# Optimization experiments

Measured on AMD Instinct MI355X. Metric: run time of the kernel, lower is better.

Reference implementation:

```python
import jax, jax.numpy as jnp
import numpy as np

T, B, E, H, HID, SIG = 1024, 4, 1024, 16, 1024, 64


def setup_inputs() -> dict:
    key = jax.random.key(0)
    ks = jax.random.split(key, 16)
    sc = 0.02
    return {
        "x": jax.random.normal(ks[0], (T, B, E), jnp.float32),
        "Wq": jax.random.normal(ks[1], (E, E), jnp.float32) * sc,
        "bq": jnp.zeros((E,), jnp.float32),
        "Wk": jax.random.normal(ks[2], (E, E), jnp.float32) * sc,
        "bk": jnp.zeros((E,), jnp.float32),
        "Wv": jax.random.normal(ks[3], (E, E), jnp.float32) * sc,
        "bv": jnp.zeros((E,), jnp.float32),
        "Wo": jax.random.normal(ks[4], (E, E), jnp.float32) * sc,
        "bo": jnp.zeros((E,), jnp.float32),
        "W1": jax.random.normal(ks[5], (HID, E), jnp.float32) * sc,
        "b1": jnp.zeros((HID,), jnp.float32),
        "W2": jax.random.normal(ks[6], (SIG, HID), jnp.float32) * sc,
        "b2": jnp.zeros((SIG,), jnp.float32),
        "head_signatures": jax.random.normal(ks[7], (H, SIG), jnp.float32),
    }


def reference(x, Wq, bq, Wk, bk, Wv, bv, Wo, bo, W1, b1, W2, b2, head_signatures):
    # x: (T, B, E) fairseq layout; self-attention, no mask, eval mode (no dropout)
    T_, B_, E_ = x.shape
    H_ = head_signatures.shape[0]
    d = E_ // H_
    scaling = d ** -0.5

    q = (x @ Wq.T + bq) * scaling            # (T,B,E)
    k = x @ Wk.T + bk
    v = x @ Wv.T + bv

    def split_heads(z):                        # (T,B,E) -> (B,H,T,d)
        return z.reshape(T_, B_, H_, d).transpose(1, 2, 0, 3)

    qh, kh, vh = split_heads(q), split_heads(k), split_heads(v)

    scores = jnp.einsum("bhtd,bhsd->bhts", qh, kh)   # (B,H,T,T)
    attn = jax.nn.softmax(scores, axis=-1)
    o = jnp.einsum("bhts,bhsd->bhtd", attn, vh)      # (B,H,T,d)

    # head-competition gate: signature MLP on x, match against head signatures,
    # softmax over heads ('softmax' competition type)
    t = jax.nn.relu(x @ W1.T + b1) @ W2.T + b2       # (T,B,SIG)
    logits = t @ head_signatures.T                   # (T,B,H)
    gate = jax.nn.softmax(logits, axis=-1)
    gate = gate.transpose(1, 2, 0)                   # (B,H,T)

    o = o * gate[..., None]                          # gate per-head outputs
    out = o.transpose(2, 0, 1, 3).reshape(T_, B_, E_)  # (T,B,E)
    return out @ Wo.T + bo
```

## Files before the change

### kernel.cpp

```cpp
#include <hip/hip_runtime.h>

#define Tn   1024
#define Bn   4
#define En   1024
#define Hn   16
#define HIDn 1024
#define SIGn 64
#define Mn   (Tn * Bn)

typedef short  s8x8  __attribute__((ext_vector_type(8)));
typedef float  f32x4 __attribute__((ext_vector_type(4)));

__device__ __forceinline__ unsigned short f2bf(float f) {
    unsigned int x = __float_as_uint(f);
    unsigned int r = (x + 0x7fffu + ((x >> 16) & 1u)) >> 16;
    return (unsigned short)r;
}
__device__ __forceinline__ float exp2asm(float x) {
    float r;
    asm("v_exp_f32 %0, %1" : "=v"(r) : "v"(x));
    return r;
}
__device__ __forceinline__ unsigned int cvtpk(float a, float b) {
    unsigned int r;
    asm("v_cvt_pk_bf16_f32 %0, %1, %2" : "=v"(r) : "v"(a), "v"(b));
    return r;
}

__device__ __forceinline__ void gload_lds16(const void* g, void* l) {
    __builtin_amdgcn_global_load_lds(
        (const __attribute__((address_space(1))) unsigned int*)g,
        (__attribute__((address_space(3))) unsigned int*)l, 16, 0, 0);
}

__device__ __forceinline__ void cast8(const float* s, unsigned short* d) {
    const float4* p = (const float4*)s;
    float4 a = p[0], b = p[1];
    s8x8 o;
    o[0] = (short)f2bf(a.x); o[1] = (short)f2bf(a.y);
    o[2] = (short)f2bf(a.z); o[3] = (short)f2bf(a.w);
    o[4] = (short)f2bf(b.x); o[5] = (short)f2bf(b.y);
    o[6] = (short)f2bf(b.z); o[7] = (short)f2bf(b.w);
    *(s8x8*)d = o;
}

__global__ __launch_bounds__(256) void prep_all(
    const float* __restrict__ x,  const float* __restrict__ W1,
    const float* __restrict__ Wq, const float* __restrict__ Wk,
    const float* __restrict__ Wv, const float* __restrict__ W2,
    const float* __restrict__ b1, const float* __restrict__ bq,
    const float* __restrict__ bk, const float* __restrict__ bv,
    unsigned short* __restrict__ Wcat, unsigned short* __restrict__ W2b,
    float* __restrict__ bcat, unsigned short* __restrict__ xb, int pre)
{
    const size_t WELEM = (size_t)En * En;
    const int y = blockIdx.y, bx = blockIdx.x, tid = threadIdx.x;
    if (y < 4) {
        const float* src = (y == 0) ? W1 : (y == 1) ? Wq : (y == 2) ? Wk : Wv;
        size_t i = (size_t)bx * 256 + tid;
        cast8(src + i * 8, Wcat + y * WELEM + i * 8);
    } else if (y == 4) {
        if (bx < 32) {
            size_t i = (size_t)bx * 256 + tid;
            cast8(W2 + i * 8, W2b + i * 8);
        } else if (bx < 48) {
            int idx = (bx - 32) * 256 + tid;
            int w = idx >> 10;
            const float* s = (w == 0) ? b1 : (w == 1) ? bq : (w == 2) ? bk : bv;
            bcat[idx] = s[idx & 1023];
        }
    } else {
        if (!pre) return;
        int q = y - 5;
        size_t i = (size_t)bx * 256 + tid;
        cast8(x + q * WELEM + i * 8, xb + q * WELEM + i * 8);
    }
}

template <int PRE>
__global__ __launch_bounds__(256) void fused_proj(
    const float* __restrict__ X, const unsigned short* __restrict__ Xb,
    const unsigned short* __restrict__ Wcat, const float* __restrict__ bcat,
    unsigned short* __restrict__ t1b, unsigned short* __restrict__ qb,
    unsigned short* __restrict__ kb, unsigned short* __restrict__ vb)
{
    __shared__ __align__(16) short As[128 * 32];
    __shared__ __align__(16) short Bs[128 * 32];
    const int tid  = threadIdx.x;
    const int wave = tid >> 6;
    const int lane = tid & 63;
    const int ln15 = lane & 15;
    const int kq   = lane >> 4;
    const int wr   = wave >> 1;
    const int wc   = wave & 1;
    const int bn   = blockIdx.x;
    const int bm   = blockIdx.y;
    const size_t rowA0 = (size_t)bm * 128;
    const size_t rowB0 = (size_t)bn * 128;

    const int lrow   = lane >> 2;
    const int lchunk = lane & 3;

    f32x4 acc[4][4];
#pragma unroll
    for (int m = 0; m < 4; m++)
#pragma unroll
        for (int n = 0; n < 4; n++) acc[m][n] = (f32x4){0.f, 0.f, 0.f, 0.f};

    for (int k0 = 0; k0 < 1024; k0 += 32) {
#pragma unroll
        for (int i = 0; i < 2; i++) {
            int row = wave * 32 + i * 16 + lrow;
            int c   = lchunk ^ ((row >> 1) & 3);
            gload_lds16(Wcat + (rowB0 + row) * 1024 + k0 + c * 8,
                        &Bs[(wave * 32 + i * 16) * 32]);
        }
        if (PRE) {
#pragma unroll
            for (int i = 0; i < 2; i++) {
                int row = wave * 32 + i * 16 + lrow;
                int c   = lchunk ^ ((row >> 1) & 3);
                gload_lds16(Xb + (rowA0 + row) * 1024 + k0 + c * 8,
                            &As[(wave * 32 + i * 16) * 32]);
            }
        } else {
            const int srow = tid >> 1;
            const int scol = (tid & 1) * 16;
            const float4* src = (const float4*)(X + (rowA0 + srow) * 1024 + k0 + scol);
            float4 a = src[0], b = src[1], c4 = src[2], d4 = src[3];
            s8x8 v0, v1;
            v0[0] = (short)f2bf(a.x);  v0[1] = (short)f2bf(a.y);
            v0[2] = (short)f2bf(a.z);  v0[3] = (short)f2bf(a.w);
            v0[4] = (short)f2bf(b.x);  v0[5] = (short)f2bf(b.y);
            v0[6] = (short)f2bf(b.z);  v0[7] = (short)f2bf(b.w);
            v1[0] = (short)f2bf(c4.x); v1[1] = (short)f2bf(c4.y);
            v1[2] = (short)f2bf(c4.z); v1[3] = (short)f2bf(c4.w);
            v1[4] = (short)f2bf(d4.x); v1[5] = (short)f2bf(d4.y);
            v1[6] = (short)f2bf(d4.z); v1[7] = (short)f2bf(d4.w);
            int sw = (srow >> 1) & 3;
            int c0 = (scol >> 3) ^ sw;
            int c1 = ((scol >> 3) + 1) ^ sw;
            *(s8x8*)&As[srow * 32 + c0 * 8] = v0;
            *(s8x8*)&As[srow * 32 + c1 * 8] = v1;
        }
        asm volatile("s_waitcnt vmcnt(0)" ::: "memory");
        __syncthreads();

        s8x8 af[4], bf[4];
#pragma unroll
        for (int m = 0; m < 4; m++) {
            int row = wr * 64 + m * 16 + ln15;
            af[m] = *(const s8x8*)&As[row * 32 + (kq ^ ((row >> 1) & 3)) * 8];
        }
#pragma unroll
        for (int n = 0; n < 4; n++) {
            int row = wc * 64 + n * 16 + ln15;
            bf[n] = *(const s8x8*)&Bs[row * 32 + (kq ^ ((row >> 1) & 3)) * 8];
        }
#pragma unroll
        for (int m = 0; m < 4; m++)
#pragma unroll
            for (int n = 0; n < 4; n++)
                acc[m][n] = __builtin_amdgcn_mfma_f32_16x16x32_bf16(
                    af[m], bf[n], acc[m][n], 0, 0, 0);
        __syncthreads();
    }

    const int which = bn >> 3;
    unsigned short* dst = (which == 0) ? t1b : (which == 1) ? qb
                        : (which == 2) ? kb : vb;
    const float scale = (which == 1) ? 0.18033688011112042f : 1.0f;
    const int   relu  = (which == 0);
    const int   cbase = (bn & 7) * 128;

    float bcol[4];
#pragma unroll
    for (int n = 0; n < 4; n++)
        bcol[n] = bcat[bn * 128 + wc * 64 + n * 16 + ln15];
#pragma unroll
    for (int m = 0; m < 4; m++) {
        size_t gr0 = rowA0 + wr * 64 + m * 16 + kq * 4;
#pragma unroll
        for (int n = 0; n < 4; n++) {
            int gc = cbase + wc * 64 + n * 16 + ln15;
#pragma unroll
            for (int j = 0; j < 4; j++) {
                float vv = acc[m][n][j] + bcol[n];
                if (relu) vv = fmaxf(vv, 0.f);
                vv *= scale;
                dst[(gr0 + j) * 1024 + gc] = f2bf(vv);
            }
        }
    }
}

__global__ __launch_bounds__(256) void out_proj(
    const unsigned short* __restrict__ A, const unsigned short* __restrict__ W,
    const float* __restrict__ bias, float* __restrict__ C)
{
    __shared__ __align__(16) short As[64 * 32];
    __shared__ __align__(16) short Bs[128 * 32];
    const int tid  = threadIdx.x;
    const int wave = tid >> 6;
    const int lane = tid & 63;
    const int ln15 = lane & 15;
    const int kq   = lane >> 4;
    const int wr   = wave >> 1;
    const int wc   = wave & 1;
    const size_t rowA0 = (size_t)blockIdx.y * 64;
    const size_t rowB0 = (size_t)blockIdx.x * 128;
    const int lrow   = lane >> 2;
    const int lchunk = lane & 3;

    f32x4 acc[2][4];
#pragma unroll
    for (int m = 0; m < 2; m++)
#pragma unroll
        for (int n = 0; n < 4; n++) acc[m][n] = (f32x4){0.f, 0.f, 0.f, 0.f};

    for (int k0 = 0; k0 < 1024; k0 += 32) {
        {
            int row = wave * 16 + lrow;
            int c   = lchunk ^ ((row >> 1) & 3);
            gload_lds16(A + (rowA0 + row) * 1024 + k0 + c * 8,
                        &As[(wave * 16) * 32]);
        }
#pragma unroll
        for (int i = 0; i < 2; i++) {
            int row = wave * 32 + i * 16 + lrow;
            int c   = lchunk ^ ((row >> 1) & 3);
            gload_lds16(W + (rowB0 + row) * 1024 + k0 + c * 8,
                        &Bs[(wave * 32 + i * 16) * 32]);
        }
        asm volatile("s_waitcnt vmcnt(0)" ::: "memory");
        __syncthreads();

        s8x8 af[2], bf[4];
#pragma unroll
        for (int m = 0; m < 2; m++) {
            int row = wr * 32 + m * 16 + ln15;
            af[m] = *(const s8x8*)&As[row * 32 + (kq ^ ((row >> 1) & 3)) * 8];
        }
#pragma unroll
        for (int n = 0; n < 4; n++) {
            int row = wc * 64 + n * 16 + ln15;
            bf[n] = *(const s8x8*)&Bs[row * 32 + (kq ^ ((row >> 1) & 3)) * 8];
        }
#pragma unroll
        for (int m = 0; m < 2; m++)
#pragma unroll
            for (int n = 0; n < 4; n++)
                acc[m][n] = __builtin_amdgcn_mfma_f32_16x16x32_bf16(
                    af[m], bf[n], acc[m][n], 0, 0, 0);
        __syncthreads();
    }

    float bcol[4];
#pragma unroll
    for (int n = 0; n < 4; n++)
        bcol[n] = bias[rowB0 + wc * 64 + n * 16 + ln15];
#pragma unroll
    for (int m = 0; m < 2; m++) {
        size_t gr0 = rowA0 + wr * 32 + m * 16 + kq * 4;
#pragma unroll
        for (int n = 0; n < 4; n++) {
            size_t gc = rowB0 + wc * 64 + n * 16 + ln15;
#pragma unroll
            for (int j = 0; j < 4; j++)
                C[(gr0 + j) * 1024 + gc] = acc[m][n][j] + bcol[n];
        }
    }
}

__device__ __forceinline__ void t2gate_body(
    int blk, int tid,
    const unsigned short* __restrict__ t1, const unsigned short* __restrict__ W2b,
    const float* __restrict__ b2, const float* __restrict__ hs,
    float* __restrict__ gate,
    short* As, short* Bs, float (*t2s)[65], float (*hss)[65])
{
    const int wave  = tid >> 6;
    const int lane  = tid & 63;
    const int ln15  = lane & 15;
    const int kq    = lane >> 4;
    const int lrow8 = lane >> 3;
    const int lch   = lane & 7;
    const int m0    = blk * 16;

    {
        int r = tid >> 4, c = (tid & 15) * 4;
        float4 v = *(const float4*)(hs + r * 64 + c);
        hss[r][c] = v.x; hss[r][c + 1] = v.y; hss[r][c + 2] = v.z; hss[r][c + 3] = v.w;
    }

    f32x4 acc = (f32x4){0.f, 0.f, 0.f, 0.f};
    for (int k0 = 0; k0 < 1024; k0 += 64) {
        if (wave < 2) {
            int row = wave * 8 + lrow8;
            int cg  = lch ^ (row & 7);
            gload_lds16(t1 + (size_t)(m0 + row) * 1024 + k0 + cg * 8,
                        As + (wave * 8) * 64);
        }
#pragma unroll
        for (int i = 0; i < 2; i++) {
            int row = wave * 16 + i * 8 + lrow8;
            int cg  = lch ^ (row & 7);
            gload_lds16(W2b + (size_t)row * 1024 + k0 + cg * 8,
                        Bs + (wave * 16 + i * 8) * 64);
        }
        asm volatile("s_waitcnt vmcnt(0)" ::: "memory");
        __syncthreads();

#pragma unroll
        for (int kk = 0; kk < 2; kk++) {
            int arow = ln15;
            int brow = wave * 16 + ln15;
            s8x8 af = *(const s8x8*)(As + arow * 64 + (((kk * 4 + kq) ^ (arow & 7)) * 8));
            s8x8 bf = *(const s8x8*)(Bs + brow * 64 + (((kk * 4 + kq) ^ (brow & 7)) * 8));
            acc = __builtin_amdgcn_mfma_f32_16x16x32_bf16(af, bf, acc, 0, 0, 0);
        }
        __syncthreads();
    }

#pragma unroll
    for (int j = 0; j < 4; j++)
        t2s[kq * 4 + j][wave * 16 + ln15] = acc[j] + b2[wave * 16 + ln15];
    __syncthreads();

    int r = tid >> 4, hd = tid & 15;
    float s = 0.f;
#pragma unroll 16
    for (int d = 0; d < 64; d++) s += t2s[r][d] * hss[hd][d];
    float mx = s;
    mx = fmaxf(mx, __shfl_xor(mx, 1));
    mx = fmaxf(mx, __shfl_xor(mx, 2));
    mx = fmaxf(mx, __shfl_xor(mx, 4));
    mx = fmaxf(mx, __shfl_xor(mx, 8));
    float e = __expf(s - mx);
    float sum = e;
    sum += __shfl_xor(sum, 1);
    sum += __shfl_xor(sum, 2);
    sum += __shfl_xor(sum, 4);
    sum += __shfl_xor(sum, 8);
    gate[(size_t)(m0 + r) * Hn + hd] = e / sum;
}

__device__ __forceinline__ void vtrans_body(
    int bh, int t0, int tid,
    const unsigned short* __restrict__ vb, unsigned short* __restrict__ vt,
    unsigned short (*ts)[65])
{
    const int b = bh >> 4, h = bh & 15;
    {
        int tr = tid >> 2, dq = (tid & 3) * 16;
        const unsigned short* src =
            vb + ((size_t)(t0 + tr) * Bn + b) * En + h * 64 + dq;
        s8x8 a = *(const s8x8*)src;
        s8x8 c = *(const s8x8*)(src + 8);
#pragma unroll
        for (int i = 0; i < 8; i++) {
            ts[tr][dq + i]     = (unsigned short)a[i];
            ts[tr][dq + 8 + i] = (unsigned short)c[i];
        }
    }
    __syncthreads();
    {
        int dr = tid >> 2, tq = (tid & 3) * 16;
        unsigned short* dst = vt + ((size_t)bh * 64 + dr) * Tn + t0 + tq;
        s8x8 o0, o1;
#pragma unroll
        for (int i = 0; i < 8; i++) {
            o0[i] = (short)ts[tq + i][dr];
            o1[i] = (short)ts[tq + 8 + i][dr];
        }
        *(s8x8*)dst = o0;
        *(s8x8*)(dst + 8) = o1;
    }
}

__global__ __launch_bounds__(256) void t2gate_k(
    const unsigned short* __restrict__ t1, const unsigned short* __restrict__ W2b,
    const float* __restrict__ b2, const float* __restrict__ hs,
    float* __restrict__ gate)
{
    __shared__ __align__(16) short As[16 * 64];
    __shared__ __align__(16) short Bs[64 * 64];
    __shared__ float t2s[16][65];
    __shared__ float hss[16][65];
    t2gate_body(blockIdx.x, threadIdx.x, t1, W2b, b2, hs, gate, As, Bs, t2s, hss);
}
__global__ __launch_bounds__(256) void trans_wo_k(
    const unsigned short* __restrict__ vb, unsigned short* __restrict__ vt,
    const float* __restrict__ Wo, unsigned short* __restrict__ Wob)
{
    const int bx = blockIdx.x, tid = threadIdx.x;
    if (bx >= 1024) {
        size_t i = (size_t)(bx - 1024) * 256 + tid;
        cast8(Wo + i * 8, Wob + i * 8);
        return;
    }
    __shared__ unsigned short ts[64][65];
    vtrans_body(bx & 63, (bx >> 6) * 64, tid, vb, vt, ts);
}

__global__ __launch_bounds__(256) void midstage(
    const unsigned short* __restrict__ t1, const unsigned short* __restrict__ W2b,
    const float* __restrict__ b2, const float* __restrict__ hs,
    float* __restrict__ gate,
    const unsigned short* __restrict__ vb, unsigned short* __restrict__ vt,
    const float* __restrict__ Wo, unsigned short* __restrict__ Wob)
{
    __shared__ __align__(16) short As[16 * 64];
    __shared__ __align__(16) short Bs[64 * 64];
    __shared__ float t2s[16][65];
    __shared__ float hss[16][65];
    __shared__ unsigned short ts[64][65];
    const int bx = blockIdx.x, tid = threadIdx.x;
    if (bx < 256) {
        t2gate_body(bx, tid, t1, W2b, b2, hs, gate, As, Bs, t2s, hss);
    } else if (bx < 1280) {
        int v = bx - 256;
        vtrans_body(v & 63, (v >> 6) * 64, tid, vb, vt, ts);
    } else {
        size_t i = (size_t)(bx - 1280) * 256 + tid;
        cast8(Wo + i * 8, Wob + i * 8);
    }
}

__global__ __launch_bounds__(512, 2) void attn_mfma(
    const unsigned short* __restrict__ q, const unsigned short* __restrict__ k,
    const unsigned short* __restrict__ vt, const float* __restrict__ gate,
    unsigned short* __restrict__ o)
{
    __shared__ __align__(16) short Kls[2][64 * 64];
    __shared__ __align__(16) short Vls[2][64 * 64];

    const int tid  = threadIdx.x;
    const int w    = tid >> 6;
    const int lane = tid & 63;
    const int ln   = lane & 15;
    const int kq   = lane >> 4;
    const int bh   = blockIdx.x;
    const int b    = bh >> 4;
    const int h    = bh & 15;
    const int qt   = blockIdx.y;

    s8x8 qf[2];
    {
        const int qrow = qt * 128 + w * 16 + ln;
        const unsigned short* src =
            q + ((size_t)qrow * Bn + b) * En + h * 64 + kq * 8;
        qf[0] = *(const s8x8*)(src);
        qf[1] = *(const s8x8*)(src + 32);
    }

    f32x4 OT[4];
#pragma unroll
    for (int n = 0; n < 4; n++) OT[n] = (f32x4){0.f, 0.f, 0.f, 0.f};
    float mrun = -1e30f, lrun = 0.f;

    const int srow = w * 8 + (lane >> 3);
    const int sch  = (lane & 7) ^ (srow & 7);
    const int sn  = srow >> 4;
    const int sK0 = 32 * (sn >> 1) + 4 * (sn & 1)
                  + 8 * ((srow >> 2) & 3) + (srow & 3);

    auto stage = [&](int bufi, int s0) {
        const unsigned short* gk =
            k + ((size_t)(s0 + sK0) * Bn + b) * En + h * 64 + sch * 8;
        gload_lds16(gk, &Kls[bufi][w * 512]);
        const unsigned short* gv =
            vt + ((size_t)bh * 64 + srow) * Tn + s0 + sch * 8;
        gload_lds16(gv, &Vls[bufi][w * 512]);
    };

    stage(0, 0);
    asm volatile("s_waitcnt vmcnt(0)" ::: "memory");
    __syncthreads();

    int cur = 0;
    for (int t = 0; t < Tn / 64; t++) {
        if (t + 1 < Tn / 64) stage(cur ^ 1, (t + 1) * 64);

        f32x4 S[4];
        __builtin_amdgcn_s_setprio(1);
#pragma unroll
        for (int n = 0; n < 4; n++) {
            S[n] = (f32x4){0.f, 0.f, 0.f, 0.f};
#pragma unroll
            for (int kk = 0; kk < 2; kk++) {
                int row = n * 16 + ln;
                int cc  = (kk * 4 + kq) ^ (row & 7);
                s8x8 kf = *(const s8x8*)&Kls[cur][row * 64 + cc * 8];
                S[n] = __builtin_amdgcn_mfma_f32_16x16x32_bf16(kf, qf[kk], S[n], 0, 0, 0);
            }
        }
        __builtin_amdgcn_s_setprio(0);

        float rm;
        {
            f32x4 t0 = S[0];
#pragma unroll
            for (int n = 1; n < 4; n++) {
                t0[0] = fmaxf(t0[0], S[n][0]); t0[1] = fmaxf(t0[1], S[n][1]);
                t0[2] = fmaxf(t0[2], S[n][2]); t0[3] = fmaxf(t0[3], S[n][3]);
            }
            rm = fmaxf(fmaxf(t0[0], t0[1]), fmaxf(t0[2], t0[3]));
            rm = fmaxf(rm, __shfl_xor(rm, 16));
            rm = fmaxf(rm, __shfl_xor(rm, 32));
        }

        if (__any(rm > mrun + 8.0f)) {
            float mnew = fmaxf(mrun, rm);
            float fs = exp2asm(mrun - mnew);
            lrun *= fs;
#pragma unroll
            for (int n = 0; n < 4; n++) {
                OT[n][0] *= fs; OT[n][1] *= fs; OT[n][2] *= fs; OT[n][3] *= fs;
            }
            mrun = mnew;
        }

        float ps = 0.f;
#pragma unroll
        for (int n = 0; n < 4; n++) {
            S[n][0] = exp2asm(S[n][0] - mrun); ps += S[n][0];
            S[n][1] = exp2asm(S[n][1] - mrun); ps += S[n][1];
            S[n][2] = exp2asm(S[n][2] - mrun); ps += S[n][2];
            S[n][3] = exp2asm(S[n][3] - mrun); ps += S[n][3];
        }
        ps += __shfl_xor(ps, 16);
        ps += __shfl_xor(ps, 32);
        lrun += ps;

        union { unsigned int u[4]; s8x8 v; } pb[2];
#pragma unroll
        for (int kk = 0; kk < 2; kk++) {
            pb[kk].u[0] = cvtpk(S[2 * kk][0],     S[2 * kk][1]);
            pb[kk].u[1] = cvtpk(S[2 * kk][2],     S[2 * kk][3]);
            pb[kk].u[2] = cvtpk(S[2 * kk + 1][0], S[2 * kk + 1][1]);
            pb[kk].u[3] = cvtpk(S[2 * kk + 1][2], S[2 * kk + 1][3]);
        }

        __builtin_amdgcn_s_setprio(1);
#pragma unroll
        for (int kk = 0; kk < 2; kk++) {
#pragma unroll
            for (int n = 0; n < 4; n++) {
                int row = n * 16 + ln;
                int cv  = (kk * 4 + kq) ^ (row & 7);
                s8x8 vf = *(const s8x8*)&Vls[cur][row * 64 + cv * 8];
                OT[n] = __builtin_amdgcn_mfma_f32_16x16x32_bf16(vf, pb[kk].v, OT[n], 0, 0, 0);
            }
        }
        __builtin_amdgcn_s_setprio(0);

        asm volatile("s_waitcnt vmcnt(0)" ::: "memory");
        __syncthreads();
        cur ^= 1;
    }

    {
        int tq = qt * 128 + w * 16 + ln;
        size_t m = (size_t)tq * Bn + b;
        float g = gate[m * Hn + h] / lrun;
        unsigned short* dst = o + m * En + h * 64;
#pragma unroll
        for (int n = 0; n < 4; n++) {
            int d0 = n * 16 + kq * 4;
            uint2 pkv;
            pkv.x = cvtpk(OT[n][0] * g, OT[n][1] * g);
            pkv.y = cvtpk(OT[n][2] * g, OT[n][3] * g);
            *(uint2*)(dst + d0) = pkv;
        }
    }
}

extern "C" void kernel_launch(void* const* d_in, const int* in_sizes, int n_in,
                              void* d_out, int out_size, void* d_ws, size_t ws_size,
                              hipStream_t stream)
{
    const float* x  = (const float*)d_in[0];
    const float* Wq = (const float*)d_in[1];
    const float* bq = (const float*)d_in[2];
    const float* Wk = (const float*)d_in[3];
    const float* bk = (const float*)d_in[4];
    const float* Wv = (const float*)d_in[5];
    const float* bv = (const float*)d_in[6];
    const float* Wo = (const float*)d_in[7];
    const float* bo = (const float*)d_in[8];
    const float* W1 = (const float*)d_in[9];
    const float* b1 = (const float*)d_in[10];
    const float* W2 = (const float*)d_in[11];
    const float* b2 = (const float*)d_in[12];
    const float* hs = (const float*)d_in[13];

    const size_t WELEM = (size_t)En * En;
    unsigned short* Wcat = (unsigned short*)d_ws;
    unsigned short* W2b  = Wcat + 4 * WELEM;
    float* bcat = (float*)(W2b + (size_t)SIGn * HIDn);
    float* gate = bcat + 4096;
    unsigned short* t1b = (unsigned short*)(gate + (size_t)Mn * Hn);
    unsigned short* qb  = t1b + (size_t)Mn * En;
    unsigned short* kb  = qb  + (size_t)Mn * En;
    unsigned short* vb  = kb  + (size_t)Mn * En;
    unsigned short* xb  = vb  + (size_t)Mn * En;
    unsigned short* Wob = Wcat;
    unsigned short* ob  = vb;

    const size_t need_xb =
        (size_t)((char*)(xb + (size_t)Mn * En) - (char*)d_ws);
    const bool pre = ws_size >= need_xb;

    dim3 blk(256);

    prep_all<<<dim3(512, 9), blk, 0, stream>>>(
        x, W1, Wq, Wk, Wv, W2, b1, bq, bk, bv, Wcat, W2b, bcat, xb, (int)pre);

    if (pre) {
        unsigned short* vtb = xb;
        fused_proj<1><<<dim3(32, 32), blk, 0, stream>>>(
            x, xb, Wcat, bcat, t1b, qb, kb, vb);
        midstage<<<dim3(1792), blk, 0, stream>>>(
            t1b, W2b, b2, hs, gate, vb, vtb, Wo, Wob);
        attn_mfma<<<dim3(Bn * Hn, Tn / 128), dim3(512), 0, stream>>>(
            qb, kb, vtb, gate, ob);
    } else {
        unsigned short* vtb = t1b;
        fused_proj<0><<<dim3(32, 32), blk, 0, stream>>>(
            x, xb, Wcat, bcat, t1b, qb, kb, vb);
        t2gate_k<<<dim3(Mn / 16), blk, 0, stream>>>(t1b, W2b, b2, hs, gate);
        trans_wo_k<<<dim3(1536), blk, 0, stream>>>(vb, vtb, Wo, Wob);
        attn_mfma<<<dim3(Bn * Hn, Tn / 128), dim3(512), 0, stream>>>(
            qb, kb, vtb, gate, ob);
    }

    out_proj<<<dim3(En / 128, Mn / 64), blk, 0, stream>>>(ob, Wob, bo, (float*)d_out);
}
```

Baseline: 119.9 us.

## Rewrite fused projection GEMM with 256x256 tiles and double-buffered LDS pipeline

Replaces the pre-cast path of the fused QKV/W1 projection with a new 512-thread kernel that uses 256x256 output tiles, BK=64, and two LDS buffers. Global-to-LDS loads for stage t+2 are issued while stage t computes, with vmcnt waits and s_setprio around the MFMA block. The aim is more reuse per tile and hiding load latency. In exchange it uses much more LDS (128KB) and more accumulator registers, which lowers occupancy, and it launches only 256 blocks.

New measurement: 113.0 us, median of 2. -5.7%, faster.

```diff
diff --git a/kernel.cpp b/kernel.cpp
--- a/kernel.cpp
+++ b/kernel.cpp
@@ -77,9 +77,132 @@
     }
 }
 
-template <int PRE>
-__global__ __launch_bounds__(256) void fused_proj(
-    const float* __restrict__ X, const unsigned short* __restrict__ Xb,
+__global__ __launch_bounds__(512) void fused_proj8(
+    const unsigned short* __restrict__ Xb,
+    const unsigned short* __restrict__ Wcat, const float* __restrict__ bcat,
+    unsigned short* __restrict__ t1b, unsigned short* __restrict__ qb,
+    unsigned short* __restrict__ kb, unsigned short* __restrict__ vb)
+{
+    __shared__ __align__(16) short As[2][256 * 64];
+    __shared__ __align__(16) short Bs[2][256 * 64];
+
+    const int tid  = threadIdx.x;
+    const int w    = tid >> 6;
+    const int lane = tid & 63;
+    const int ln15 = lane & 15;
+    const int kq   = lane >> 4;
+    const int wr   = w >> 2;
+    const int wc   = w & 3;
+    const int bn   = blockIdx.x;
+    const int bm   = blockIdx.y;
+    const size_t rowA0 = (size_t)bm * 256;
+    const size_t rowB0 = (size_t)bn * 256;
+
+    const int rl = lane >> 3;
+    const int cg = (lane & 7) ^ rl;
+    const unsigned short* Abase = Xb   + (rowA0 + w * 8 + rl) * 1024 + cg * 8;
+    const unsigned short* Bbase = Wcat + (rowB0 + w * 8 + rl) * 1024 + cg * 8;
+    const int ldsW = w * 512;
+
+    f32x4 acc[8][4];
+#pragma unroll
+    for (int m = 0; m < 8; m++)
+#pragma unroll
+        for (int n = 0; n < 4; n++) acc[m][n] = (f32x4){0.f, 0.f, 0.f, 0.f};
+
+    auto STG = [&](int buf, int k0) {
+#pragma unroll
+        for (int i = 0; i < 4; i++)
+            gload_lds16(Abase + (size_t)i * 64 * 1024 + k0,
+                        &As[buf][i * 4096 + ldsW]);
+#pragma unroll
+        for (int i = 0; i < 4; i++)
+            gload_lds16(Bbase + (size_t)i * 64 * 1024 + k0,
+                        &Bs[buf][i * 4096 + ldsW]);
+    };
+
+    auto COMPUTE = [&](const short* lA, const short* lB) {
+#pragma unroll
+        for (int q = 0; q < 4; q++) {
+            const int rh = q >> 1, ch = q & 1;
+            s8x8 af[4][2], bf[2][2];
+#pragma unroll
+            for (int m = 0; m < 2 + 2; m++) {
+                int row = wr * 128 + (rh * 4 + m) * 16 + ln15;
+#pragma unroll
+                for (int kk = 0; kk < 2; kk++)
+                    af[m][kk] = *(const s8x8*)&lA[row * 64 +
+                        (((kk * 4 + kq) ^ (row & 7)) * 8)];
+            }
+#pragma unroll
+            for (int n = 0; n < 2; n++) {
+                int row = wc * 64 + (ch * 2 + n) * 16 + ln15;
+#pragma unroll
+                for (int kk = 0; kk < 2; kk++)
+                    bf[n][kk] = *(const s8x8*)&lB[row * 64 +
+                        (((kk * 4 + kq) ^ (row & 7)) * 8)];
+            }
+            __builtin_amdgcn_s_setprio(1);
+#pragma unroll
+            for (int m = 0; m < 4; m++)
+#pragma unroll
+                for (int n = 0; n < 2; n++)
+#pragma unroll
+                    for (int kk = 0; kk < 2; kk++)
+                        acc[rh * 4 + m][ch * 2 + n] =
+                            __builtin_amdgcn_mfma_f32_16x16x32_bf16(
+                                af[m][kk], bf[n][kk],
+                                acc[rh * 4 + m][ch * 2 + n], 0, 0, 0);
+            __builtin_amdgcn_s_setprio(0);
+        }
+    };
+
+    STG(0, 0);
+    STG(1, 64);
+
+    for (int t = 0; t < 16; t++) {
+        if (t < 15)
+            asm volatile("s_waitcnt vmcnt(8)" ::: "memory");
+        else
+            asm volatile("s_waitcnt vmcnt(0)" ::: "memory");
+        __builtin_amdgcn_s_barrier();
+        asm volatile("" ::: "memory");
+        COMPUTE(&As[t & 1][0], &Bs[t & 1][0]);
+        asm volatile("" ::: "memory");
+        __builtin_amdgcn_s_barrier();
+        if (t + 2 < 16) STG(t & 1, (t + 2) * 64);
+    }
+
+    const int which = bn >> 2;
+    unsigned short* dst = (which == 0) ? t1b : (which == 1) ? qb
+                        : (which == 2) ? kb : vb;
+    const float scale = (which == 1) ? 0.18033688011112042f : 1.0f;
+    const int   relu  = (which == 0);
+    const int   cbase = (bn & 3) * 256;
+
+    float bcol[4];
+#pragma unroll
+    for (int n = 0; n < 4; n++)
+        bcol[n] = bcat[bn * 256 + wc * 64 + n * 16 + ln15];
+#pragma unroll
+    for (int m = 0; m < 8; m++) {
+        size_t gr0 = rowA0 + wr * 128 + m * 16 + kq * 4;
+#pragma unroll
+        for (int n = 0; n < 4; n++) {
+            int gc = cbase + wc * 64 + n * 16 + ln15;
+#pragma unroll
+            for (int j = 0; j < 4; j++) {
+                float vv = acc[m][n][j] + bcol[n];
+                if (relu) vv = fmaxf(vv, 0.f);
+                vv *= scale;
+                dst[(gr0 + j) * 1024 + gc] = f2bf(vv);
+            }
+        }
+    }
+}
+
+__global__ __launch_bounds__(256) void fused_proj_fb(
+    const float* __restrict__ X,
     const unsigned short* __restrict__ Wcat, const float* __restrict__ bcat,
     unsigned short* __restrict__ t1b, unsigned short* __restrict__ qb,
     unsigned short* __restrict__ kb, unsigned short* __restrict__ vb)
@@ -97,7 +220,6 @@
     const int bm   = blockIdx.y;
     const size_t rowA0 = (size_t)bm * 128;
     const size_t rowB0 = (size_t)bn * 128;
-
     const int lrow   = lane >> 2;
     const int lchunk = lane & 3;
 
@@ -115,15 +237,7 @@
             gload_lds16(Wcat + (rowB0 + row) * 1024 + k0 + c * 8,
                         &Bs[(wave * 32 + i * 16) * 32]);
         }
-        if (PRE) {
-#pragma unroll
-            for (int i = 0; i < 2; i++) {
-                int row = wave * 32 + i * 16 + lrow;
-                int c   = lchunk ^ ((row >> 1) & 3);
-                gload_lds16(Xb + (rowA0 + row) * 1024 + k0 + c * 8,
-                            &As[(wave * 32 + i * 16) * 32]);
-            }
-        } else {
+        {
             const int srow = tid >> 1;
             const int scol = (tid & 1) * 16;
             const float4* src = (const float4*)(X + (rowA0 + srow) * 1024 + k0 + scol);
@@ -619,16 +733,16 @@
 
     if (pre) {
         unsigned short* vtb = xb;
-        fused_proj<1><<<dim3(32, 32), blk, 0, stream>>>(
-            x, xb, Wcat, bcat, t1b, qb, kb, vb);
+        fused_proj8<<<dim3(16, 16), dim3(512), 0, stream>>>(
+            xb, Wcat, bcat, t1b, qb, kb, vb);
         midstage<<<dim3(1792), blk, 0, stream>>>(
             t1b, W2b, b2, hs, gate, vb, vtb, Wo, Wob);
         attn_mfma<<<dim3(Bn * Hn, Tn / 128), dim3(512), 0, stream>>>(
             qb, kb, vtb, gate, ob);
     } else {
         unsigned short* vtb = t1b;
-        fused_proj<0><<<dim3(32, 32), blk, 0, stream>>>(
-            x, xb, Wcat, bcat, t1b, qb, kb, vb);
+        fused_proj_fb<<<dim3(32, 32), blk, 0, stream>>>(
+            x, Wcat, bcat, t1b, qb, kb, vb);
         t2gate_k<<<dim3(Mn / 16), blk, 0, stream>>>(t1b, W2b, b2, hs, gate);
         trans_wo_k<<<dim3(1536), blk, 0, stream>>>(vb, vtb, Wo, Wob);
         attn_mfma<<<dim3(Bn * Hn, Tn / 128), dim3(512), 0, stream>>>(
```
